# Kernel tuning notes

Measured on AMD Instinct MI355X. Metric: run time of the kernel, lower is better.

The kernel has to match this reference:

```python
import jax, jax.numpy as jnp
import numpy as np

FILTER_LENGTH = 1024
HOP_LENGTH = 512
CUTOFF = FILTER_LENGTH // 2 + 1  # 513
PAD = FILTER_LENGTH // 2         # 512
BATCH = 32
NUM_SAMPLES = 524288


def _make_forward_basis():
    # DFT matrix: fft of identity -> rows are DFT basis vectors
    fb = np.fft.fft(np.eye(FILTER_LENGTH))
    basis = np.vstack([np.real(fb[:CUTOFF, :]), np.imag(fb[:CUTOFF, :])])  # [1026, 1024]
    # periodic ('fftbins=True') Hann window of length filter_length
    n = np.arange(FILTER_LENGTH)
    window = 0.5 - 0.5 * np.cos(2.0 * np.pi * n / FILTER_LENGTH)
    return (basis * window).astype(np.float32)


def setup_inputs() -> dict:
    key = jax.random.key(0)
    input_data = jax.random.normal(key, (BATCH, NUM_SAMPLES), dtype=jnp.float32)
    forward_basis = jnp.asarray(_make_forward_basis())  # [1026, 1024]
    return {"input_data": input_data, "forward_basis": forward_basis}


def reference(input_data, forward_basis):
    # reflect-pad by filter_length/2 on both sides of the time axis
    x = jnp.pad(input_data, ((0, 0), (PAD, PAD)), mode="reflect")[:, None, :]  # [B,1,L+2P]
    kernel = forward_basis[:, None, :]  # [out=1026, in=1, k=1024]
    # strided conv1d == windowed DFT matmul against dense Fourier basis
    ft = jax.lax.conv_general_dilated(
        x, kernel,
        window_strides=(HOP_LENGTH,),
        padding="VALID",
        dimension_numbers=("NCH", "OIH", "NCH"),
    )  # [B, 1026, T]
    real = ft[:, :CUTOFF, :]
    imag = ft[:, CUTOFF:, :]
    magnitude = jnp.sqrt(real * real + imag * imag)  # [B, 513, T]
    return magnitude
```

## Files before the change

kernel.cpp:

```cpp
#include <hip/hip_runtime.h>
#include <math.h>

#define NSAMP 524288
#define NTOT  32800
#define OUTB  525825
#define FPB   16

__device__ __forceinline__ void fft8(float (&xr)[8], float (&xi)[8]) {
    const float S2 = 0.70710678118654752f;
    float t0r = xr[0] + xr[4], t0i = xi[0] + xi[4];
    float t1r = xr[0] - xr[4], t1i = xi[0] - xi[4];
    float t2r = xr[2] + xr[6], t2i = xi[2] + xi[6];
    float t3r = xr[2] - xr[6], t3i = xi[2] - xi[6];
    float E0r = t0r + t2r, E0i = t0i + t2i;
    float E2r = t0r - t2r, E2i = t0i - t2i;
    float E1r = t1r + t3i, E1i = t1i - t3r;
    float E3r = t1r - t3i, E3i = t1i + t3r;
    float u0r = xr[1] + xr[5], u0i = xi[1] + xi[5];
    float u1r = xr[1] - xr[5], u1i = xi[1] - xi[5];
    float u2r = xr[3] + xr[7], u2i = xi[3] + xi[7];
    float u3r = xr[3] - xr[7], u3i = xi[3] - xi[7];
    float O0r = u0r + u2r, O0i = u0i + u2i;
    float O2r = u0r - u2r, O2i = u0i - u2i;
    float O1r = u1r + u3i, O1i = u1i - u3r;
    float O3r = u1r - u3i, O3i = u1i + u3r;
    float w1r = S2 * (O1r + O1i), w1i = S2 * (O1i - O1r);
    float w2r = O2i,              w2i = -O2r;
    float w3r = S2 * (O3i - O3r), w3i = -S2 * (O3r + O3i);
    xr[0] = E0r + O0r; xi[0] = E0i + O0i;
    xr[4] = E0r - O0r; xi[4] = E0i - O0i;
    xr[1] = E1r + w1r; xi[1] = E1i + w1i;
    xr[5] = E1r - w1r; xi[5] = E1i - w1i;
    xr[2] = E2r + w2r; xi[2] = E2i + w2i;
    xr[6] = E2r - w2r; xi[6] = E2i - w2i;
    xr[3] = E3r + w3r; xi[3] = E3i + w3i;
    xr[7] = E3r - w3r; xi[7] = E3i - w3i;
}

__global__ __launch_bounds__(256) void stft_fft_kernel(
    const float* __restrict__ x, float* __restrict__ out)
{
    __shared__ float scr[4][1184];
    __shared__ float obuf[513 * 17];

    const int tid = threadIdx.x;
    const int wave = tid >> 6, l = tid & 63;
    float* S = scr[wave];
    const int gt0 = blockIdx.x * FPB;
    const float PI = 3.14159265358979f;

    for (int it = 0; it < 4; ++it) {
        const int tloc = wave * 4 + it;
        const int gt = gt0 + tloc;
        const int b = gt / 1025;
        const int t = gt - b * 1025;
        const float* __restrict__ xb = x + (size_t)b * NSAMP;
        const int sbase = t * 512 - 512;

        float cr[8], ci[8];
        float c1, s1;
        __sincosf(PI * (float)l * (1.0f / 256.0f), &s1, &c1);

        asm volatile("s_waitcnt lgkmcnt(0)" ::: "memory");

        {
            float cs = c1, sn = s1;
            const float CD = 0.9999811753f, SD = 0.0061358846f;
            const float C4 = 0.70710678f;
            const bool edge = (t == 0) || (t == 1024);
#pragma unroll
            for (int n1 = 0; n1 < 8; ++n1) {
                const int n = 2 * (l + 64 * n1);
                float xe, xo;
                if (!edge) {
                    const float2 v = *reinterpret_cast<const float2*>(xb + sbase + n);
                    xe = v.x; xo = v.y;
                } else {
                    int sa = sbase + n, sb2 = sbase + n + 1;
                    if (sa < 0) sa = -sa;
                    if (sa >= NSAMP) sa = 2 * (NSAMP - 1) - sa;
                    if (sb2 < 0) sb2 = -sb2;
                    if (sb2 >= NSAMP) sb2 = 2 * (NSAMP - 1) - sb2;
                    xe = xb[sa]; xo = xb[sb2];
                }
                const float we = 0.5f - 0.5f * cs;
                const float cso = cs * CD - sn * SD;
                const float wo = 0.5f - 0.5f * cso;
                cr[n1] = xe * we;
                ci[n1] = xo * wo;
                const float cn = cs * C4 - sn * C4;
                sn = sn * C4 + cs * C4;
                cs = cn;
            }
        }

        fft8(cr, ci);

        {
            float wr = c1, wi = -s1;
#pragma unroll
            for (int k = 1; k < 8; ++k) {
                const float rr = cr[k] * wr - ci[k] * wi;
                const float ii = cr[k] * wi + ci[k] * wr;
                cr[k] = rr; ci[k] = ii;
                const float nwr = wr * c1 + wi * s1;
                const float nwi = wi * c1 - wr * s1;
                wr = nwr; wi = nwi;
            }
        }

#pragma unroll
        for (int k = 0; k < 8; ++k) { S[k * 72 + l] = cr[k]; S[576 + k * 72 + l] = ci[k]; }
        asm volatile("s_waitcnt lgkmcnt(0)" ::: "memory");
        const int kap = l >> 3, m2 = l & 7;
#pragma unroll
        for (int m1 = 0; m1 < 8; ++m1) {
            cr[m1] = S[kap * 72 + 8 * m1 + m2];
            ci[m1] = S[576 + kap * 72 + 8 * m1 + m2];
        }
        asm volatile("s_waitcnt lgkmcnt(0)" ::: "memory");

        fft8(cr, ci);

        {
            float cb, sb;
            __sincosf(PI * (float)m2 * (1.0f / 32.0f), &sb, &cb);
            float wr = cb, wi = -sb;
#pragma unroll
            for (int j = 1; j < 8; ++j) {
                const float rr = cr[j] * wr - ci[j] * wi;
                const float ii = cr[j] * wi + ci[j] * wr;
                cr[j] = rr; ci[j] = ii;
                const float nwr = wr * cb + wi * sb;
                const float nwi = wi * cb - wr * sb;
                wr = nwr; wi = nwi;
            }
        }

#pragma unroll
        for (int j = 0; j < 8; ++j) {
            S[j * 72 + 8 * m2 + kap] = cr[j];
            S[576 + j * 72 + 8 * m2 + kap] = ci[j];
        }
        asm volatile("s_waitcnt lgkmcnt(0)" ::: "memory");
        const int j1 = l & 7;
#pragma unroll
        for (int m = 0; m < 8; ++m) {
            cr[m] = S[j1 * 72 + 8 * m + kap];
            ci[m] = S[576 + j1 * 72 + 8 * m + kap];
        }
        asm volatile("s_waitcnt lgkmcnt(0)" ::: "memory");

        fft8(cr, ci);

#pragma unroll
        for (int j2 = 0; j2 < 8; ++j2) {
            const int k = kap + 8 * j1 + 64 * j2;
            S[k] = cr[j2]; S[576 + k] = ci[j2];
        }
        asm volatile("s_waitcnt lgkmcnt(0)" ::: "memory");

        {
            float cbb, sbb;
            __sincosf(PI * (float)l * (1.0f / 512.0f), &sbb, &cbb);
            float wr = cbb, wi = -sbb;
            const float CS8 = 0.9238795325f, SN8 = 0.3826834324f;
#pragma unroll
            for (int r = 0; r < 8; ++r) {
                const int k = l + 64 * r;
                const int k2 = (512 - k) & 511;
                const float Zer = S[k],  Zei = S[576 + k];
                const float Zor = S[k2], Zoi = S[576 + k2];
                const float Ar = 0.5f * (Zer + Zor);
                const float Ai = 0.5f * (Zei - Zoi);
                const float Br = 0.5f * (Zei + Zoi);
                const float Bi = 0.5f * (Zor - Zer);
                const float Xr = Ar + Br * wr - Bi * wi;
                const float Xi = Ai + Br * wi + Bi * wr;
                obuf[k * 17 + tloc] = sqrtf(Xr * Xr + Xi * Xi);
                const float nwr = wr * CS8 + wi * SN8;
                const float nwi = wi * CS8 - wr * SN8;
                wr = nwr; wi = nwi;
            }
            if (l == 0) obuf[512 * 17 + tloc] = fabsf(S[0] - S[576]);
        }
    }

    __syncthreads();

    const int kk = tid >> 4, c = tid & 15;
    const int gtc = gt0 + c;
    const int bc = gtc / 1025, tc = gtc - bc * 1025;
    const size_t oaddr = (size_t)bc * OUTB + tc;
#pragma unroll
    for (int p = 0; p < 33; ++p) {
        const int k = p * 16 + kk;
        if (k < 513) out[oaddr + (size_t)k * 1025] = obuf[k * 17 + c];
    }
}

extern "C" void kernel_launch(void* const* d_in, const int* in_sizes, int n_in,
                              void* d_out, int out_size, void* d_ws, size_t ws_size,
                              hipStream_t stream) {
    const float* x = (const float*)d_in[0];
    float* out = (float*)d_out;
    stft_fft_kernel<<<NTOT / FPB, 256, 0, stream>>>(x, out);
}
```

Baseline: 158.9 us.

## Process two frames per wave and precompute window and twiddle tables in registers

Each wave now handles two STFT frames at once, giving each its own LDS scratch region so their loads, FFT stages and LDS transposes interleave for more instruction-level parallelism. Window coefficients and all three twiddle sets are computed once per thread before the loop and kept in registers, so they are no longer recomputed for every frame. The explicit s_waitcnt barriers are dropped in favour of compiler-managed waits, and launch bounds now request 2 blocks per CU. The price is higher register pressure from the twiddle arrays plus two frames in flight, and double the per-wave LDS scratch, either of which could cut occupancy or cause spills.

Result: no change. 155.8 us (-1.9%).

```diff
diff --git a/kernel.cpp b/kernel.cpp
--- a/kernel.cpp
+++ b/kernel.cpp
@@ -37,152 +37,208 @@
     xr[7] = E3r - w3r; xi[7] = E3i - w3i;
 }
 
-__global__ __launch_bounds__(256) void stft_fft_kernel(
+__global__ __launch_bounds__(256, 2) void stft_fft_kernel(
     const float* __restrict__ x, float* __restrict__ out)
 {
-    __shared__ float scr[4][1184];
+    __shared__ float scr[4][2][1184];
     __shared__ float obuf[513 * 17];
 
     const int tid = threadIdx.x;
     const int wave = tid >> 6, l = tid & 63;
-    float* S = scr[wave];
+    const int kap = l >> 3, m2 = l & 7, j1 = l & 7;
     const int gt0 = blockIdx.x * FPB;
     const float PI = 3.14159265358979f;
 
-    for (int it = 0; it < 4; ++it) {
-        const int tloc = wave * 4 + it;
-        const int gt = gt0 + tloc;
-        const int b = gt / 1025;
-        const int t = gt - b * 1025;
-        const float* __restrict__ xb = x + (size_t)b * NSAMP;
-        const int sbase = t * 512 - 512;
-
-        float cr[8], ci[8];
-        float c1, s1;
-        __sincosf(PI * (float)l * (1.0f / 256.0f), &s1, &c1);
-
-        asm volatile("s_waitcnt lgkmcnt(0)" ::: "memory");
-
-        {
-            float cs = c1, sn = s1;
-            const float CD = 0.9999811753f, SD = 0.0061358846f;
-            const float C4 = 0.70710678f;
-            const bool edge = (t == 0) || (t == 1024);
-#pragma unroll
-            for (int n1 = 0; n1 < 8; ++n1) {
-                const int n = 2 * (l + 64 * n1);
-                float xe, xo;
-                if (!edge) {
-                    const float2 v = *reinterpret_cast<const float2*>(xb + sbase + n);
-                    xe = v.x; xo = v.y;
-                } else {
-                    int sa = sbase + n, sb2 = sbase + n + 1;
+    float c1, s1;
+    __sincosf(PI * (float)l * (1.0f / 256.0f), &s1, &c1);
+
+    float wea[8], woa[8];
+    {
+        const float CD = 0.9999811753f, SD = 0.0061358846f;
+        const float C4 = 0.70710678f;
+        float cs = c1, sn = s1;
+#pragma unroll
+        for (int n1 = 0; n1 < 8; ++n1) {
+            wea[n1] = 0.5f - 0.5f * cs;
+            const float cso = cs * CD - sn * SD;
+            woa[n1] = 0.5f - 0.5f * cso;
+            const float cn = cs * C4 - sn * C4;
+            sn = sn * C4 + cs * C4;
+            cs = cn;
+        }
+    }
+    float w1r[8], w1i[8];
+    {
+        float wr = c1, wi = -s1;
+#pragma unroll
+        for (int k = 1; k < 8; ++k) {
+            w1r[k] = wr; w1i[k] = wi;
+            const float nwr = wr * c1 + wi * s1;
+            const float nwi = wi * c1 - wr * s1;
+            wr = nwr; wi = nwi;
+        }
+    }
+    float w2r[8], w2i[8];
+    {
+        float cb, sb;
+        __sincosf(PI * (float)m2 * (1.0f / 32.0f), &sb, &cb);
+        float wr = cb, wi = -sb;
+#pragma unroll
+        for (int j = 1; j < 8; ++j) {
+            w2r[j] = wr; w2i[j] = wi;
+            const float nwr = wr * cb + wi * sb;
+            const float nwi = wi * cb - wr * sb;
+            wr = nwr; wi = nwi;
+        }
+    }
+    float w3r[8], w3i[8];
+    {
+        float cbb, sbb;
+        __sincosf(PI * (float)l * (1.0f / 512.0f), &sbb, &cbb);
+        const float CS8 = 0.9238795325f, SN8 = 0.3826834324f;
+        float wr = cbb, wi = -sbb;
+#pragma unroll
+        for (int r = 0; r < 8; ++r) {
+            w3r[r] = wr; w3i[r] = wi;
+            const float nwr = wr * CS8 + wi * SN8;
+            const float nwi = wi * CS8 - wr * SN8;
+            wr = nwr; wi = nwi;
+        }
+    }
+
+    for (int it = 0; it < 2; ++it) {
+        float cr[2][8], ci[2][8];
+        int tl[2]; const float* xbp[2]; int sb0[2]; bool edge[2];
+#pragma unroll
+        for (int p = 0; p < 2; ++p) {
+            const int tloc = wave * 4 + it * 2 + p;
+            const int gt = gt0 + tloc;
+            const int b = gt / 1025;
+            const int t = gt - b * 1025;
+            tl[p] = tloc;
+            xbp[p] = x + (size_t)b * NSAMP;
+            sb0[p] = t * 512 - 512;
+            edge[p] = (t == 0) || (t == 1024);
+        }
+
+#pragma unroll
+        for (int p = 0; p < 2; ++p) {
+            if (!edge[p]) {
+#pragma unroll
+                for (int n1 = 0; n1 < 8; ++n1) {
+                    const float2 v = *reinterpret_cast<const float2*>(
+                        xbp[p] + sb0[p] + 2 * (l + 64 * n1));
+                    cr[p][n1] = v.x; ci[p][n1] = v.y;
+                }
+            } else {
+#pragma unroll
+                for (int n1 = 0; n1 < 8; ++n1) {
+                    const int n = 2 * (l + 64 * n1);
+                    int sa = sb0[p] + n, sb2 = sb0[p] + n + 1;
                     if (sa < 0) sa = -sa;
                     if (sa >= NSAMP) sa = 2 * (NSAMP - 1) - sa;
                     if (sb2 < 0) sb2 = -sb2;
                     if (sb2 >= NSAMP) sb2 = 2 * (NSAMP - 1) - sb2;
-                    xe = xb[sa]; xo = xb[sb2];
+                    cr[p][n1] = xbp[p][sa]; ci[p][n1] = xbp[p][sb2];
                 }
-                const float we = 0.5f - 0.5f * cs;
-                const float cso = cs * CD - sn * SD;
-                const float wo = 0.5f - 0.5f * cso;
-                cr[n1] = xe * we;
-                ci[n1] = xo * wo;
-                const float cn = cs * C4 - sn * C4;
-                sn = sn * C4 + cs * C4;
-                cs = cn;
-            }
-        }
-
-        fft8(cr, ci);
-
-        {
-            float wr = c1, wi = -s1;
+            }
+        }
+#pragma unroll
+        for (int p = 0; p < 2; ++p)
+#pragma unroll
+            for (int n1 = 0; n1 < 8; ++n1) {
+                cr[p][n1] *= wea[n1]; ci[p][n1] *= woa[n1];
+            }
+
+        fft8(cr[0], ci[0]); fft8(cr[1], ci[1]);
+
+#pragma unroll
+        for (int p = 0; p < 2; ++p)
 #pragma unroll
             for (int k = 1; k < 8; ++k) {
-                const float rr = cr[k] * wr - ci[k] * wi;
-                const float ii = cr[k] * wi + ci[k] * wr;
-                cr[k] = rr; ci[k] = ii;
-                const float nwr = wr * c1 + wi * s1;
-                const float nwi = wi * c1 - wr * s1;
-                wr = nwr; wi = nwi;
-            }
-        }
-
-#pragma unroll
-        for (int k = 0; k < 8; ++k) { S[k * 72 + l] = cr[k]; S[576 + k * 72 + l] = ci[k]; }
-        asm volatile("s_waitcnt lgkmcnt(0)" ::: "memory");
-        const int kap = l >> 3, m2 = l & 7;
-#pragma unroll
-        for (int m1 = 0; m1 < 8; ++m1) {
-            cr[m1] = S[kap * 72 + 8 * m1 + m2];
-            ci[m1] = S[576 + kap * 72 + 8 * m1 + m2];
-        }
-        asm volatile("s_waitcnt lgkmcnt(0)" ::: "memory");
-
-        fft8(cr, ci);
-
-        {
-            float cb, sb;
-            __sincosf(PI * (float)m2 * (1.0f / 32.0f), &sb, &cb);
-            float wr = cb, wi = -sb;
+                const float rr = cr[p][k] * w1r[k] - ci[p][k] * w1i[k];
+                const float ii = cr[p][k] * w1i[k] + ci[p][k] * w1r[k];
+                cr[p][k] = rr; ci[p][k] = ii;
+            }
+
+#pragma unroll
+        for (int p = 0; p < 2; ++p) {
+            float* P = scr[wave][p];
+#pragma unroll
+            for (int k = 0; k < 8; ++k) {
+                P[k * 72 + l] = cr[p][k];
+                P[576 + k * 72 + l] = ci[p][k];
+            }
+        }
+#pragma unroll
+        for (int p = 0; p < 2; ++p) {
+            float* P = scr[wave][p];
+#pragma unroll
+            for (int m1 = 0; m1 < 8; ++m1) {
+                cr[p][m1] = P[kap * 72 + 8 * m1 + m2];
+                ci[p][m1] = P[576 + kap * 72 + 8 * m1 + m2];
+            }
+        }
+
+        fft8(cr[0], ci[0]); fft8(cr[1], ci[1]);
+
+#pragma unroll
+        for (int p = 0; p < 2; ++p)
 #pragma unroll
             for (int j = 1; j < 8; ++j) {
-                const float rr = cr[j] * wr - ci[j] * wi;
-                const float ii = cr[j] * wi + ci[j] * wr;
-                cr[j] = rr; ci[j] = ii;
-                const float nwr = wr * cb + wi * sb;
-                const float nwi = wi * cb - wr * sb;
-                wr = nwr; wi = nwi;
-            }
-        }
-
-#pragma unroll
-        for (int j = 0; j < 8; ++j) {
-            S[j * 72 + 8 * m2 + kap] = cr[j];
-            S[576 + j * 72 + 8 * m2 + kap] = ci[j];
-        }
-        asm volatile("s_waitcnt lgkmcnt(0)" ::: "memory");
-        const int j1 = l & 7;
-#pragma unroll
-        for (int m = 0; m < 8; ++m) {
-            cr[m] = S[j1 * 72 + 8 * m + kap];
-            ci[m] = S[576 + j1 * 72 + 8 * m + kap];
-        }
-        asm volatile("s_waitcnt lgkmcnt(0)" ::: "memory");
-
-        fft8(cr, ci);
-
-#pragma unroll
-        for (int j2 = 0; j2 < 8; ++j2) {
-            const int k = kap + 8 * j1 + 64 * j2;
-            S[k] = cr[j2]; S[576 + k] = ci[j2];
-        }
-        asm volatile("s_waitcnt lgkmcnt(0)" ::: "memory");
-
-        {
-            float cbb, sbb;
-            __sincosf(PI * (float)l * (1.0f / 512.0f), &sbb, &cbb);
-            float wr = cbb, wi = -sbb;
-            const float CS8 = 0.9238795325f, SN8 = 0.3826834324f;
+                const float rr = cr[p][j] * w2r[j] - ci[p][j] * w2i[j];
+                const float ii = cr[p][j] * w2i[j] + ci[p][j] * w2r[j];
+                cr[p][j] = rr; ci[p][j] = ii;
+            }
+
+#pragma unroll
+        for (int p = 0; p < 2; ++p) {
+            float* P = scr[wave][p];
+#pragma unroll
+            for (int j = 0; j < 8; ++j) {
+                P[j * 72 + 8 * m2 + kap] = cr[p][j];
+                P[576 + j * 72 + 8 * m2 + kap] = ci[p][j];
+            }
+        }
+#pragma unroll
+        for (int p = 0; p < 2; ++p) {
+            float* P = scr[wave][p];
+#pragma unroll
+            for (int m = 0; m < 8; ++m) {
+                cr[p][m] = P[j1 * 72 + 8 * m + kap];
+                ci[p][m] = P[576 + j1 * 72 + 8 * m + kap];
+            }
+        }
+
+        fft8(cr[0], ci[0]); fft8(cr[1], ci[1]);
+
+#pragma unroll
+        for (int p = 0; p < 2; ++p) {
+            float* P = scr[wave][p];
+#pragma unroll
+            for (int j2 = 0; j2 < 8; ++j2) {
+                const int k = kap + 8 * j1 + 64 * j2;
+                P[k] = cr[p][j2]; P[576 + k] = ci[p][j2];
+            }
+        }
+#pragma unroll
+        for (int p = 0; p < 2; ++p) {
+            float* P = scr[wave][p];
 #pragma unroll
             for (int r = 0; r < 8; ++r) {
                 const int k = l + 64 * r;
                 const int k2 = (512 - k) & 511;
-                const float Zer = S[k],  Zei = S[576 + k];
-                const float Zor = S[k2], Zoi = S[576 + k2];
+                const float Zer = P[k],  Zei = P[576 + k];
+                const float Zor = P[k2], Zoi = P[576 + k2];
                 const float Ar = 0.5f * (Zer + Zor);
                 const float Ai = 0.5f * (Zei - Zoi);
                 const float Br = 0.5f * (Zei + Zoi);
                 const float Bi = 0.5f * (Zor - Zer);
-                const float Xr = Ar + Br * wr - Bi * wi;
-                const float Xi = Ai + Br * wi + Bi * wr;
-                obuf[k * 17 + tloc] = sqrtf(Xr * Xr + Xi * Xi);
-                const float nwr = wr * CS8 + wi * SN8;
-                const float nwi = wi * CS8 - wr * SN8;
-                wr = nwr; wi = nwi;
-            }
-            if (l == 0) obuf[512 * 17 + tloc] = fabsf(S[0] - S[576]);
+                const float Xr = Ar + Br * w3r[r] - Bi * w3i[r];
+                const float Xi = Ai + Br * w3i[r] + Bi * w3r[r];
+                obuf[k * 17 + tl[p]] = sqrtf(Xr * Xr + Xi * Xi);
+            }
+            if (l == 0) obuf[512 * 17 + tl[p]] = fabsf(P[0] - P[576]);
         }
     }
 
```
